# Kernel optimization log

Hardware: AMD Instinct MI355X
Metric: run time of the kernel (lower is better)

The kernel has to match this reference:

```python
import jax, jax.numpy as jnp
import numpy as np

H = 1024
B = 8
T = 2048

def setup_inputs() -> dict:
    key = jax.random.key(0)
    ks = jax.random.split(key, 12)
    s = 1.0 / np.sqrt(H)
    return {
        "x": jax.random.normal(ks[0], (B, T, H), dtype=jnp.float32),
        "time_decay": jax.random.normal(ks[1], (H,), dtype=jnp.float32) * 0.1,
        "time_first": jax.random.normal(ks[2], (H,), dtype=jnp.float32) * 0.1,
        "time_mix_key": jax.random.uniform(ks[3], (1, 1, H), dtype=jnp.float32),
        "time_mix_value": jax.random.uniform(ks[4], (1, 1, H), dtype=jnp.float32),
        "time_mix_receptance": jax.random.uniform(ks[5], (1, 1, H), dtype=jnp.float32),
        "Wk": jax.random.normal(ks[6], (H, H), dtype=jnp.float32) * s,
        "Wv": jax.random.normal(ks[7], (H, H), dtype=jnp.float32) * s,
        "Wr": jax.random.normal(ks[8], (H, H), dtype=jnp.float32) * s,
        "Wo": jax.random.normal(ks[9], (H, H), dtype=jnp.float32) * s,
        "bo": jax.random.normal(ks[10], (H,), dtype=jnp.float32) * 0.01,
    }

def reference(x, time_decay, time_first, time_mix_key, time_mix_value,
              time_mix_receptance, Wk, Wv, Wr, Wo, bo):
    # time shift: shifted[:, t] = x[:, t-1], shifted[:, 0] = 0
    shifted = jnp.pad(x, ((0, 0), (1, 0), (0, 0)))[:, :-1]
    k_in = x * time_mix_key + shifted * (1.0 - time_mix_key)
    v_in = x * time_mix_value + shifted * (1.0 - time_mix_value)
    r_in = x * time_mix_receptance + shifted * (1.0 - time_mix_receptance)
    k = jnp.einsum('bth,oh->bto', k_in, Wk)
    v = jnp.einsum('bth,oh->bto', v_in, Wv)
    r = jax.nn.sigmoid(jnp.einsum('bth,oh->bto', r_in, Wr))

    td = jnp.exp(-jnp.exp(time_decay))  # (H,)

    def step(carry, kv):
        num, den = carry            # (B, H) each
        k_t, v_t = kv               # (B, H) each
        e = jnp.exp(time_first + k_t)
        out_t = (num + e * v_t) / (den + e)
        ek = jnp.exp(k_t)
        return (td * num + ek * v_t, td * den + ek), out_t

    init = (jnp.zeros((x.shape[0], x.shape[2]), x.dtype),
            jnp.zeros((x.shape[0], x.shape[2]), x.dtype))
    # scan over time: (T, B, H)
    _, wkv = jax.lax.scan(step, init, (k.transpose(1, 0, 2), v.transpose(1, 0, 2)))
    wkv = wkv.transpose(1, 0, 2)    # (B, T, H)

    return jnp.einsum('bth,oh->bto', r * wkv, Wo) + bo
```

## Files before the change

### kernel.cpp

```cpp
#include <hip/hip_runtime.h>
#include <hip/hip_bf16.h>
#include <cstdint>
#include <cstddef>

#define HH 1024
#define BB 8
#define TT 2048
#define MM (BB*TT)
#define CC 64
#define LL (TT/CC)

typedef __attribute__((ext_vector_type(8))) short bf16x8;
typedef __attribute__((ext_vector_type(4))) float f32x4;

__device__ __forceinline__ unsigned short f2bf(float f) {
  union { float f; unsigned u; } v; v.f = f;
  return (unsigned short)((v.u + 0x7fffu + ((v.u >> 16) & 1u)) >> 16);
}
__device__ __forceinline__ float bf2f(unsigned short s) {
  union { float f; unsigned u; } v; v.u = ((unsigned)s) << 16;
  return v.f;
}

__device__ __forceinline__ void load_lds16(const void* g, void* l) {
  __builtin_amdgcn_global_load_lds((const __attribute__((address_space(1))) void*)g,
                                   (__attribute__((address_space(3))) void*)l,
                                   16, 0, 0);
}

__global__ __launch_bounds__(256) void conv_w(const float* __restrict__ Wk,
    const float* __restrict__ Wv, const float* __restrict__ Wr,
    const float* __restrict__ Wo, unsigned short* __restrict__ dst) {
  const int i = (blockIdx.x * 256 + threadIdx.x) * 4;
  const float* src = blockIdx.y == 0 ? Wk : blockIdx.y == 1 ? Wv : blockIdx.y == 2 ? Wr : Wo;
  const float4 v = *(const float4*)(src + i);
  ushort4 o; o.x = f2bf(v.x); o.y = f2bf(v.y); o.z = f2bf(v.z); o.w = f2bf(v.w);
  *(ushort4*)(dst + (size_t)blockIdx.y * HH * HH + i) = o;
}

__global__ __launch_bounds__(256) void mix_kernel(const float* __restrict__ x,
    const float* __restrict__ tmk, const float* __restrict__ tmv, const float* __restrict__ tmr,
    unsigned short* __restrict__ kin, unsigned short* __restrict__ vin,
    unsigned short* __restrict__ rin) {
  const int gid = blockIdx.x * 256 + threadIdx.x;
  const size_t e0 = (size_t)gid * 4;
  const int h = (int)(e0 & (HH - 1));
  const int t = (int)((e0 >> 10) & (TT - 1));
  const float4 xv = *(const float4*)(x + e0);
  float4 sv = make_float4(0.f, 0.f, 0.f, 0.f);
  if (t != 0) sv = *(const float4*)(x + e0 - HH);
  const float4 k4 = *(const float4*)(tmk + h);
  const float4 v4 = *(const float4*)(tmv + h);
  const float4 r4 = *(const float4*)(tmr + h);
  ushort4 ko, vo, ro;
  ko.x = f2bf(sv.x + k4.x * (xv.x - sv.x)); ko.y = f2bf(sv.y + k4.y * (xv.y - sv.y));
  ko.z = f2bf(sv.z + k4.z * (xv.z - sv.z)); ko.w = f2bf(sv.w + k4.w * (xv.w - sv.w));
  vo.x = f2bf(sv.x + v4.x * (xv.x - sv.x)); vo.y = f2bf(sv.y + v4.y * (xv.y - sv.y));
  vo.z = f2bf(sv.z + v4.z * (xv.z - sv.z)); vo.w = f2bf(sv.w + v4.w * (xv.w - sv.w));
  ro.x = f2bf(sv.x + r4.x * (xv.x - sv.x)); ro.y = f2bf(sv.y + r4.y * (xv.y - sv.y));
  ro.z = f2bf(sv.z + r4.z * (xv.z - sv.z)); ro.w = f2bf(sv.w + r4.w * (xv.w - sv.w));
  *(ushort4*)(kin + e0) = ko;
  *(ushort4*)(vin + e0) = vo;
  *(ushort4*)(rin + e0) = ro;
}


#define BAR()   do { asm volatile("" ::: "memory"); __builtin_amdgcn_s_barrier(); \
                     asm volatile("" ::: "memory"); } while (0)
#define LGKM0() asm volatile("s_waitcnt lgkmcnt(0)" ::: "memory")
#define VM6()   asm volatile("s_waitcnt vmcnt(6)" ::: "memory")
#define VM0()   asm volatile("s_waitcnt vmcnt(0)" ::: "memory")

__device__ __forceinline__ void stA(const unsigned short* __restrict__ Ag, int m0, int kt,
                                    unsigned short* buf, int h, int w, int rl, int scol) {
#pragma unroll
  for (int l = 0; l < 2; ++l) {
    const int row = l * 128 + h * 64 + w * 8;
    load_lds16(Ag + (size_t)(m0 + row + rl) * HH + kt + scol, buf + row * 64);
  }
}
__device__ __forceinline__ void stB(const unsigned short* __restrict__ Bg, int n0, int kt,
                                    unsigned short* buf, int h, int w, int rl, int scol) {
#pragma unroll
  for (int l = 0; l < 2; ++l) {
    const int row = (2 * (l * 2 + (w >> 2)) + h) * 32 + (w & 3) * 8;
    load_lds16(Bg + (size_t)(n0 + row + rl) * HH + kt + scol, buf + row * 64);
  }
}

template<int MH>
__device__ __forceinline__ void rdA(const unsigned short* buf, bf16x8 (&af)[4][2],
                                    int wm, int l15, int kq, int swz) {
#pragma unroll
  for (int fm = 0; fm < 4; ++fm)
#pragma unroll
    for (int kk = 0; kk < 2; ++kk)
      af[fm][kk] = *(const bf16x8*)(buf + (wm * 128 + MH * 64 + fm * 16 + l15) * 64
                                        + ((kk * 32 + kq * 8) ^ swz));
}
template<int NH>
__device__ __forceinline__ void rdB(const unsigned short* buf, bf16x8 (&bfr)[2][2][2],
                                    int wn, int l15, int kq, int swz) {
#pragma unroll
  for (int fn = 0; fn < 2; ++fn)
#pragma unroll
    for (int kk = 0; kk < 2; ++kk)
      bfr[NH][fn][kk] = *(const bf16x8*)(buf + (wn * 64 + NH * 32 + fn * 16 + l15) * 64
                                             + ((kk * 32 + kq * 8) ^ swz));
}
template<int MH, int NH>
__device__ __forceinline__ void mfmaQ(f32x4 (&acc)[8][4], const bf16x8 (&af)[4][2],
                                      const bf16x8 (&bfr)[2][2][2]) {
  __builtin_amdgcn_s_setprio(1);
#pragma unroll
  for (int kk = 0; kk < 2; ++kk)
#pragma unroll
    for (int fm = 0; fm < 4; ++fm)
#pragma unroll
      for (int fn = 0; fn < 2; ++fn)
        acc[MH * 4 + fm][NH * 2 + fn] = __builtin_amdgcn_mfma_f32_16x16x32_bf16(
            af[fm][kk], bfr[NH][fn][kk], acc[MH * 4 + fm][NH * 2 + fn], 0, 0, 0);
  __builtin_amdgcn_s_setprio(0);
}

__device__ __forceinline__ void gemm256(const unsigned short* __restrict__ Ag,
                                        const unsigned short* __restrict__ Bg,
                                        const int m0, const int n0,
                                        unsigned short* As, unsigned short* Bs,
                                        f32x4 (&acc)[8][4]) {
  const int tid = threadIdx.x;
  const int lane = tid & 63;
  const int w = tid >> 6;
  const int wm = w >> 2, wn = w & 3;
  const int l15 = lane & 15, kq = lane >> 4;
  const int swz = ((lane >> 2) & 1) << 4;
  const int rl = lane >> 3;
  const int scol = ((lane & 7) * 8) ^ (((lane >> 5) & 1) << 4);
  unsigned short* const A0 = As;
  unsigned short* const A1 = As + 256 * 64;
  unsigned short* const B0 = Bs;
  unsigned short* const B1 = Bs + 256 * 64;
  bf16x8 af[4][2], bfr[2][2][2];

  stA(Ag, m0, 0, A0, 0, w, rl, scol);
  stB(Bg, n0, 0, B0, 0, w, rl, scol);
  stB(Bg, n0, 0, B0, 1, w, rl, scol);
  stA(Ag, m0, 0, A0, 1, w, rl, scol);
  stA(Ag, m0, 64, A1, 0, w, rl, scol);
  stB(Bg, n0, 64, B1, 0, w, rl, scol);
  stB(Bg, n0, 64, B1, 1, w, rl, scol);
  VM6(); BAR();

#pragma unroll 1
  for (int i = 0; i < 8; ++i) {
    const int tb1 = ((2 * i + 1) * 64) & (HH - 1);
    const int tn0 = ((2 * i + 2) * 64) & (HH - 1);
    const int tn1 = ((2 * i + 3) * 64) & (HH - 1);
    rdA<0>(A0, af, wm, l15, kq, swz); rdB<0>(B0, bfr, wn, l15, kq, swz);
    stA(Ag, m0, tb1, A1, 1, w, rl, scol);
    BAR(); LGKM0(); mfmaQ<0, 0>(acc, af, bfr); BAR();
    rdB<1>(B0, bfr, wn, l15, kq, swz);
    stA(Ag, m0, tn0, A0, 0, w, rl, scol);
    BAR(); LGKM0(); mfmaQ<0, 1>(acc, af, bfr); BAR();
    rdA<1>(A0, af, wm, l15, kq, swz);
    stB(Bg, n0, tn0, B0, 0, w, rl, scol);
    BAR(); LGKM0(); mfmaQ<1, 1>(acc, af, bfr); BAR();
    stB(Bg, n0, tn0, B0, 1, w, rl, scol);
    VM6(); BAR(); LGKM0(); mfmaQ<1, 0>(acc, af, bfr); BAR();
    rdA<0>(A1, af, wm, l15, kq, swz); rdB<0>(B1, bfr, wn, l15, kq, swz);
    stA(Ag, m0, tn0, A0, 1, w, rl, scol);
    BAR(); LGKM0(); mfmaQ<0, 0>(acc, af, bfr); BAR();
    rdB<1>(B1, bfr, wn, l15, kq, swz);
    stA(Ag, m0, tn1, A1, 0, w, rl, scol);
    BAR(); LGKM0(); mfmaQ<0, 1>(acc, af, bfr); BAR();
    rdA<1>(A1, af, wm, l15, kq, swz);
    stB(Bg, n0, tn1, B1, 0, w, rl, scol);
    BAR(); LGKM0(); mfmaQ<1, 1>(acc, af, bfr); BAR();
    stB(Bg, n0, tn1, B1, 1, w, rl, scol);
    VM6(); BAR(); LGKM0(); mfmaQ<1, 0>(acc, af, bfr); BAR();
  }
  VM0();
}

__device__ __forceinline__ void swizzle_mn256(int x, int& m0, int& n0) {
  const int wg = (x & 7) * 32 + (x >> 3);
  m0 = (wg >> 2) * 256;
  n0 = (wg & 3) * 256;
}

__global__ __launch_bounds__(512, 2) void gemm_kvr(const unsigned short* __restrict__ kin,
    const unsigned short* __restrict__ vin, const unsigned short* __restrict__ rin,
    const unsigned short* __restrict__ Wbf,
    unsigned short* __restrict__ kb, unsigned short* __restrict__ vb,
    unsigned short* __restrict__ rb) {
  __shared__ unsigned short As[2 * 256 * 64];
  __shared__ unsigned short Bs[2 * 256 * 64];
  const int z = blockIdx.y;
  const unsigned short* Ag = z == 0 ? kin : (z == 1 ? vin : rin);
  const unsigned short* Bg = Wbf + (size_t)z * HH * HH;
  unsigned short* Cg = z == 0 ? kb : (z == 1 ? vb : rb);
  int m0, n0; swizzle_mn256(blockIdx.x, m0, n0);
  f32x4 acc[8][4] = {};
  gemm256(Ag, Bg, m0, n0, As, Bs, acc);
  const int lane = threadIdx.x & 63, w = threadIdx.x >> 6;
  const int wm = w >> 2, wn = w & 3, l15 = lane & 15, lq = lane >> 4;
  const bool sig = (z == 2);
#pragma unroll
  for (int fm = 0; fm < 8; ++fm)
#pragma unroll
    for (int fn = 0; fn < 4; ++fn) {
      const int col = n0 + wn * 64 + fn * 16 + l15;
      const int r0 = m0 + wm * 128 + fm * 16 + lq * 4;
#pragma unroll
      for (int j = 0; j < 4; ++j) {
        float vv = acc[fm][fn][j];
        if (sig) vv = 1.0f / (1.0f + __expf(-vv));
        Cg[(size_t)(r0 + j) * HH + col] = f2bf(vv);
      }
    }
}

__global__ __launch_bounds__(512, 2) void gemm_o(const unsigned short* __restrict__ Ag,
    const unsigned short* __restrict__ Bg, const float* __restrict__ bias,
    float* __restrict__ C) {
  __shared__ unsigned short As[2 * 256 * 64];
  __shared__ unsigned short Bs[2 * 256 * 64];
  int m0, n0; swizzle_mn256(blockIdx.x, m0, n0);
  f32x4 acc[8][4] = {};
  gemm256(Ag, Bg, m0, n0, As, Bs, acc);
  const int lane = threadIdx.x & 63, w = threadIdx.x >> 6;
  const int wm = w >> 2, wn = w & 3, l15 = lane & 15, lq = lane >> 4;
#pragma unroll
  for (int fm = 0; fm < 8; ++fm)
#pragma unroll
    for (int fn = 0; fn < 4; ++fn) {
      const int col = n0 + wn * 64 + fn * 16 + l15;
      const float bv = bias[col];
      const int r0 = m0 + wm * 128 + fm * 16 + lq * 4;
#pragma unroll
      for (int j = 0; j < 4; ++j)
        C[(size_t)(r0 + j) * HH + col] = acc[fm][fn][j] + bv;
    }
}

__global__ __launch_bounds__(256) void wkv_part(const unsigned short* __restrict__ k,
    const unsigned short* __restrict__ v, const float* __restrict__ tdec,
    float* __restrict__ pnum, float* __restrict__ pden) {
  const int gid = blockIdx.x * 256 + threadIdx.x;
  const int h = gid & (HH - 1);
  const int bh = gid & (BB * HH - 1);
  const int b = (gid >> 10) & (BB - 1);
  const int c = gid >> 13;
  const float td = __expf(-__expf(tdec[h]));
  size_t idx = (size_t)b * TT * HH + (size_t)(c * LL) * HH + h;
  float num = 0.f, den = 0.f;
#pragma unroll 8
  for (int i = 0; i < LL; ++i, idx += HH) {
    const float ek = __expf(bf2f(k[idx]));
    const float vt = bf2f(v[idx]);
    num = td * num + ek * vt;
    den = td * den + ek;
  }
  pnum[(size_t)c * (BB * HH) + bh] = num;
  pden[(size_t)c * (BB * HH) + bh] = den;
}

__global__ __launch_bounds__(256) void wkv_scan(const float* __restrict__ tdec,
    float* __restrict__ pnum, float* __restrict__ pden) {
  const int bh = blockIdx.x * 256 + threadIdx.x;
  const int h = bh & (HH - 1);
  const float ed = __expf(tdec[h]);
  const float tdL = __expf(-ed * (float)LL);
  float num = 0.f, den = 0.f;
#pragma unroll 8
  for (int c = 0; c < CC; ++c) {
    const size_t o = (size_t)c * (BB * HH) + bh;
    const float tn = pnum[o], td_ = pden[o];
    pnum[o] = num; pden[o] = den;
    num = tdL * num + tn;
    den = tdL * den + td_;
  }
}

__global__ __launch_bounds__(256) void wkv_final(const unsigned short* __restrict__ k,
    const unsigned short* __restrict__ v, const unsigned short* __restrict__ r,
    const float* __restrict__ tdec, const float* __restrict__ tfst,
    const float* __restrict__ pnum, const float* __restrict__ pden,
    unsigned short* __restrict__ rwkv) {
  const int gid = blockIdx.x * 256 + threadIdx.x;
  const int h = gid & (HH - 1);
  const int bh = gid & (BB * HH - 1);
  const int b = (gid >> 10) & (BB - 1);
  const int c = gid >> 13;
  const float td = __expf(-__expf(tdec[h]));
  const float etf = __expf(tfst[h]);
  float num = pnum[(size_t)c * (BB * HH) + bh];
  float den = pden[(size_t)c * (BB * HH) + bh];
  size_t idx = (size_t)b * TT * HH + (size_t)(c * LL) * HH + h;
#pragma unroll 4
  for (int i = 0; i < LL; ++i, idx += HH) {
    const float ek = __expf(bf2f(k[idx]));
    const float vt = bf2f(v[idx]);
    const float rt = bf2f(r[idx]);
    const float e = ek * etf;
    const float inv = __builtin_amdgcn_rcpf(den + e);
    const float outv = (num + e * vt) * inv;
    num = td * num + ek * vt;
    den = td * den + ek;
    rwkv[idx] = f2bf(outv * rt);
  }
}

extern "C" void kernel_launch(void* const* d_in, const int* in_sizes, int n_in,
                              void* d_out, int out_size, void* d_ws, size_t ws_size,
                              hipStream_t stream) {
  (void)in_sizes; (void)n_in; (void)out_size; (void)ws_size;
  const float* x    = (const float*)d_in[0];
  const float* tdec = (const float*)d_in[1];
  const float* tfst = (const float*)d_in[2];
  const float* tmk  = (const float*)d_in[3];
  const float* tmv  = (const float*)d_in[4];
  const float* tmr  = (const float*)d_in[5];
  const float* Wk   = (const float*)d_in[6];
  const float* Wv   = (const float*)d_in[7];
  const float* Wr   = (const float*)d_in[8];
  const float* Wo   = (const float*)d_in[9];
  const float* bo   = (const float*)d_in[10];
  float* out = (float*)d_out;

  char* ws = (char*)d_ws;
  const size_t MiB = (size_t)1 << 20;
  unsigned short* Wbf = (unsigned short*)(ws);
  unsigned short* kin = (unsigned short*)(ws + 8 * MiB);
  unsigned short* vin = (unsigned short*)(ws + 40 * MiB);
  unsigned short* rin = (unsigned short*)(ws + 72 * MiB);
  unsigned short* rb  = (unsigned short*)(ws + 104 * MiB);
  unsigned short* kb = (unsigned short*)out;
  unsigned short* vb = kb + (size_t)MM * HH;
  unsigned short* rwkv = kin;
  float* pnum = (float*)(ws + 40 * MiB);
  float* pden = (float*)(ws + 42 * MiB);

  hipLaunchKernelGGL(conv_w, dim3(1024, 4), dim3(256), 0, stream, Wk, Wv, Wr, Wo, Wbf);
  hipLaunchKernelGGL(mix_kernel, dim3(16384), dim3(256), 0, stream,
                     x, tmk, tmv, tmr, kin, vin, rin);
  hipLaunchKernelGGL(gemm_kvr, dim3(256, 3), dim3(512), 0, stream,
                     kin, vin, rin, Wbf, kb, vb, rb);
  hipLaunchKernelGGL(wkv_part, dim3(2048), dim3(256), 0, stream,
                     kb, vb, tdec, pnum, pden);
  hipLaunchKernelGGL(wkv_scan, dim3(32), dim3(256), 0, stream,
                     tdec, pnum, pden);
  hipLaunchKernelGGL(wkv_final, dim3(2048), dim3(256), 0, stream,
                     kb, vb, rb, tdec, tfst, pnum, pden, rwkv);
  hipLaunchKernelGGL(gemm_o, dim3(256), dim3(512), 0, stream,
                     rwkv, Wbf + (size_t)3 * HH * HH, bo, out);
}
```

Baseline: 363.1 us.

## Vectorize WKV passes to eight channels per thread and double chunk count

The chunked WKV partial and final kernels now have each thread handle eight adjacent channels, using 16-byte vector loads and stores of the bf16 k, v, r and output instead of 2-byte scalar accesses. The chunk count doubles so there is still enough parallelism with eight times fewer threads, and the pden buffer is moved to fit the larger partial arrays. The GEMM LDS read swizzle also gains an extra XOR bit to reduce bank conflicts. Costs are more registers per thread and a longer serial scan over chunks.

```diff
diff --git a/kernel.cpp b/kernel.cpp
--- a/kernel.cpp
+++ b/kernel.cpp
@@ -7,10 +7,11 @@
 #define BB 8
 #define TT 2048
 #define MM (BB*TT)
-#define CC 64
+#define CC 128
 #define LL (TT/CC)
 
 typedef __attribute__((ext_vector_type(8))) short bf16x8;
+typedef __attribute__((ext_vector_type(8))) unsigned short u16x8;
 typedef __attribute__((ext_vector_type(4))) float f32x4;
 
 __device__ __forceinline__ unsigned short f2bf(float f) {
@@ -133,9 +134,9 @@
   const int w = tid >> 6;
   const int wm = w >> 2, wn = w & 3;
   const int l15 = lane & 15, kq = lane >> 4;
-  const int swz = ((lane >> 2) & 1) << 4;
+  const int swz = (((lane >> 2) & 1) << 4) | (((lane >> 3) & 1) << 5);
   const int rl = lane >> 3;
-  const int scol = ((lane & 7) * 8) ^ (((lane >> 5) & 1) << 4);
+  const int scol = (((lane & 7) * 8) ^ (((lane >> 5) & 1) << 4)) ^ ((w & 1) << 5);
   unsigned short* const A0 = As;
   unsigned short* const A1 = As + 256 * 64;
   unsigned short* const B0 = Bs;
@@ -247,22 +248,30 @@
     const unsigned short* __restrict__ v, const float* __restrict__ tdec,
     float* __restrict__ pnum, float* __restrict__ pden) {
   const int gid = blockIdx.x * 256 + threadIdx.x;
-  const int h = gid & (HH - 1);
-  const int bh = gid & (BB * HH - 1);
-  const int b = (gid >> 10) & (BB - 1);
-  const int c = gid >> 13;
-  const float td = __expf(-__expf(tdec[h]));
-  size_t idx = (size_t)b * TT * HH + (size_t)(c * LL) * HH + h;
-  float num = 0.f, den = 0.f;
-#pragma unroll 8
+  const int h0 = (gid & 127) * 8;
+  const int b = (gid >> 7) & (BB - 1);
+  const int c = gid >> 10;
+  float td[8], num[8], den[8];
+#pragma unroll
+  for (int j = 0; j < 8; ++j) {
+    td[j] = __expf(-__expf(tdec[h0 + j]));
+    num[j] = 0.f; den[j] = 0.f;
+  }
+  size_t idx = (size_t)b * TT * HH + (size_t)(c * LL) * HH + h0;
+#pragma unroll 4
   for (int i = 0; i < LL; ++i, idx += HH) {
-    const float ek = __expf(bf2f(k[idx]));
-    const float vt = bf2f(v[idx]);
-    num = td * num + ek * vt;
-    den = td * den + ek;
-  }
-  pnum[(size_t)c * (BB * HH) + bh] = num;
-  pden[(size_t)c * (BB * HH) + bh] = den;
+    const u16x8 k8 = *(const u16x8*)(k + idx);
+    const u16x8 v8 = *(const u16x8*)(v + idx);
+#pragma unroll
+    for (int j = 0; j < 8; ++j) {
+      const float ek = __expf(bf2f(k8[j]));
+      num[j] = td[j] * num[j] + ek * bf2f(v8[j]);
+      den[j] = td[j] * den[j] + ek;
+    }
+  }
+  const size_t o = (size_t)c * (BB * HH) + b * HH + h0;
+#pragma unroll
+  for (int j = 0; j < 8; ++j) { pnum[o + j] = num[j]; pden[o + j] = den[j]; }
 }
 
 __global__ __launch_bounds__(256) void wkv_scan(const float* __restrict__ tdec,
@@ -288,26 +297,37 @@
     const float* __restrict__ pnum, const float* __restrict__ pden,
     unsigned short* __restrict__ rwkv) {
   const int gid = blockIdx.x * 256 + threadIdx.x;
-  const int h = gid & (HH - 1);
-  const int bh = gid & (BB * HH - 1);
-  const int b = (gid >> 10) & (BB - 1);
-  const int c = gid >> 13;
-  const float td = __expf(-__expf(tdec[h]));
-  const float etf = __expf(tfst[h]);
-  float num = pnum[(size_t)c * (BB * HH) + bh];
-  float den = pden[(size_t)c * (BB * HH) + bh];
-  size_t idx = (size_t)b * TT * HH + (size_t)(c * LL) * HH + h;
-#pragma unroll 4
+  const int h0 = (gid & 127) * 8;
+  const int b = (gid >> 7) & (BB - 1);
+  const int c = gid >> 10;
+  float td[8], etf[8], num[8], den[8];
+  const size_t o = (size_t)c * (BB * HH) + b * HH + h0;
+#pragma unroll
+  for (int j = 0; j < 8; ++j) {
+    td[j] = __expf(-__expf(tdec[h0 + j]));
+    etf[j] = __expf(tfst[h0 + j]);
+    num[j] = pnum[o + j]; den[j] = pden[o + j];
+  }
+  size_t idx = (size_t)b * TT * HH + (size_t)(c * LL) * HH + h0;
+#pragma unroll 2
   for (int i = 0; i < LL; ++i, idx += HH) {
-    const float ek = __expf(bf2f(k[idx]));
-    const float vt = bf2f(v[idx]);
-    const float rt = bf2f(r[idx]);
-    const float e = ek * etf;
-    const float inv = __builtin_amdgcn_rcpf(den + e);
-    const float outv = (num + e * vt) * inv;
-    num = td * num + ek * vt;
-    den = td * den + ek;
-    rwkv[idx] = f2bf(outv * rt);
+    const u16x8 k8 = *(const u16x8*)(k + idx);
+    const u16x8 v8 = *(const u16x8*)(v + idx);
+    const u16x8 r8 = *(const u16x8*)(r + idx);
+    u16x8 o8;
+#pragma unroll
+    for (int j = 0; j < 8; ++j) {
+      const float ek = __expf(bf2f(k8[j]));
+      const float vt = bf2f(v8[j]);
+      const float rt = bf2f(r8[j]);
+      const float e = ek * etf[j];
+      const float inv = __builtin_amdgcn_rcpf(den[j] + e);
+      const float outv = (num[j] + e * vt) * inv;
+      num[j] = td[j] * num[j] + ek * vt;
+      den[j] = td[j] * den[j] + ek;
+      o8[j] = f2bf(outv * rt);
+    }
+    *(u16x8*)(rwkv + idx) = o8;
   }
 }
 
@@ -339,18 +359,18 @@
   unsigned short* vb = kb + (size_t)MM * HH;
   unsigned short* rwkv = kin;
   float* pnum = (float*)(ws + 40 * MiB);
-  float* pden = (float*)(ws + 42 * MiB);
+  float* pden = (float*)(ws + 44 * MiB);
 
   hipLaunchKernelGGL(conv_w, dim3(1024, 4), dim3(256), 0, stream, Wk, Wv, Wr, Wo, Wbf);
   hipLaunchKernelGGL(mix_kernel, dim3(16384), dim3(256), 0, stream,
                      x, tmk, tmv, tmr, kin, vin, rin);
   hipLaunchKernelGGL(gemm_kvr, dim3(256, 3), dim3(512), 0, stream,
                      kin, vin, rin, Wbf, kb, vb, rb);
-  hipLaunchKernelGGL(wkv_part, dim3(2048), dim3(256), 0, stream,
+  hipLaunchKernelGGL(wkv_part, dim3(512), dim3(256), 0, stream,
                      kb, vb, tdec, pnum, pden);
   hipLaunchKernelGGL(wkv_scan, dim3(32), dim3(256), 0, stream,
                      tdec, pnum, pden);
-  hipLaunchKernelGGL(wkv_final, dim3(2048), dim3(256), 0, stream,
+  hipLaunchKernelGGL(wkv_final, dim3(512), dim3(256), 0, stream,
                      kb, vb, rb, tdec, tfst, pnum, pden, rwkv);
   hipLaunchKernelGGL(gemm_o, dim3(256), dim3(512), 0, stream,
                      rwkv, Wbf + (size_t)3 * HH * HH, bo, out);
```

Measured after the change: 370.7 us. +2.1%, slower.
